# Performance work log

Hardware: AMD Instinct MI355X
Metric: run time of the kernel (lower is better)

Reference implementation:

```python
import jax, jax.numpy as jnp
import numpy as np

N = 100000      # nodes
E = 3200000     # edges
H = 128         # hidden_dim
L = 2           # relation_layers
R = 8           # num_edge_types
NT = 12         # num_node_types
CARDS = [100, 50, 20]
CE = 8          # categorical_embedding_dim
NUM, BOOL = 32, 16
FH = 48         # feature_hidden_dim
HH = 64         # head_hidden_dim
NBIN = 3        # approval, destination, simulation
NSEV = 4        # severity classes
COMB = 3 * H + FH
FEAT_IN = NUM + BOOL + len(CARDS) * CE


def setup_inputs() -> dict:
    key = jax.random.key(0)
    ks = jax.random.split(key, 32)
    s = 0.05
    inp = {
        'node_type_ids': jax.random.randint(ks[0], (N,), 0, NT),
        'edge_index': jax.random.randint(ks[1], (E, 2), 0, N),
        'edge_type_ids': jax.random.randint(ks[2], (E,), 0, R),
        'categorical': jax.random.randint(ks[3], (3,), 0, 20),
        'anchor_index': 0,
        'numeric': jax.random.normal(ks[4], (NUM,), jnp.float32),
        'boolean': (jax.random.uniform(ks[5], (BOOL,)) < 0.5).astype(jnp.float32),
        'node_emb': jax.random.normal(ks[6], (NT, H), jnp.float32) * s,
        'self_W': jax.random.normal(ks[7], (L, H, H), jnp.float32) * s,
        'self_b': jax.random.normal(ks[8], (L, H), jnp.float32) * s,
        'rel_W': jax.random.normal(ks[9], (L, R, H, H), jnp.float32) * s,
        'cat_emb0': jax.random.normal(ks[10], (CARDS[0], CE), jnp.float32) * s,
        'cat_emb1': jax.random.normal(ks[11], (CARDS[1], CE), jnp.float32) * s,
        'cat_emb2': jax.random.normal(ks[12], (CARDS[2], CE), jnp.float32) * s,
        'feat_W': jax.random.normal(ks[13], (FH, FEAT_IN), jnp.float32) * s,
        'feat_b': jax.random.normal(ks[14], (FH,), jnp.float32) * s,
        'bin_W1': jax.random.normal(ks[15], (NBIN, HH, COMB), jnp.float32) * s,
        'bin_b1': jax.random.normal(ks[16], (NBIN, HH), jnp.float32) * s,
        'bin_W2': jax.random.normal(ks[17], (NBIN, 1, HH), jnp.float32) * s,
        'bin_b2': jax.random.normal(ks[18], (NBIN, 1), jnp.float32) * s,
        'mc_W1': jax.random.normal(ks[19], (HH, COMB), jnp.float32) * s,
        'mc_b1': jax.random.normal(ks[20], (HH,), jnp.float32) * s,
        'mc_W2': jax.random.normal(ks[21], (NSEV, HH), jnp.float32) * s,
        'mc_b2': jax.random.normal(ks[22], (NSEV,), jnp.float32) * s,
    }
    return inp


def reference(node_type_ids, edge_index, edge_type_ids, categorical, anchor_index,
              numeric, boolean, node_emb, self_W, self_b, rel_W,
              cat_emb0, cat_emb1, cat_emb2, feat_W, feat_b,
              bin_W1, bin_b1, bin_W2, bin_b2, mc_W1, mc_b1, mc_W2, mc_b2):
    x = node_emb[node_type_ids]                      # [N,H]
    src, tgt = edge_index[:, 0], edge_index[:, 1]
    n, h = x.shape
    r = rel_W.shape[1]
    # scatter-add of (W_r @ x_src) == W_r @ scatter-add(x_src) per (target, relation)
    seg = tgt * r + edge_type_ids                    # combined segment id
    for l in range(self_W.shape[0]):
        agg = jax.ops.segment_sum(x[src], seg, num_segments=n * r).reshape(n, r, h)
        msgs = jnp.einsum('nrh,rdh->nd', agg, rel_W[l])   # Linear (no bias): x @ W^T
        x = jax.nn.relu(x @ self_W[l].T + self_b[l] + msgs)
    anchor = x[anchor_index]
    gmean = x.mean(axis=0)
    gmax = x.max(axis=0)
    feat = jnp.concatenate([numeric, boolean,
                            cat_emb0[categorical[0]], cat_emb1[categorical[1]],
                            cat_emb2[categorical[2]]])
    enc = jax.nn.relu(feat @ feat_W.T + feat_b)      # dropout = identity (eval)
    comb = jnp.concatenate([anchor, gmean, gmax, enc])   # [COMB]
    h_bin = jax.nn.relu(jnp.einsum('khc,c->kh', bin_W1, comb) + bin_b1)
    bin_logits = (jnp.einsum('koh,kh->ko', bin_W2, h_bin) + bin_b2)[:, 0]  # [NBIN]
    h_mc = jax.nn.relu(mc_W1 @ comb + mc_b1)
    mc_logits = mc_W2 @ h_mc + mc_b2                 # [NSEV]
    return bin_logits, mc_logits
```

## Files before the change

### kernel.cpp

```cpp
#include <hip/hip_runtime.h>
#include <hip/hip_bf16.h>


#define NN 100000
#define EE 3200000

typedef __attribute__((ext_vector_type(8))) short bf16x8;
typedef __attribute__((ext_vector_type(4))) float f32x4;

static __device__ __forceinline__ float frelu(float v) { return v > 0.f ? v : 0.f; }

static __device__ __forceinline__ unsigned short f2bf(float f) {
    unsigned b = __float_as_uint(f);
    return (unsigned short)((b + 0x7fffu + ((b >> 16) & 1u)) >> 16);
}
static __device__ __forceinline__ unsigned packbf(float lo, float hi) {
    return (unsigned)f2bf(lo) | ((unsigned)f2bf(hi) << 16);
}
static __device__ __forceinline__ float bflo(unsigned u) { return __uint_as_float(u << 16); }
static __device__ __forceinline__ float bfhi(unsigned u) { return __uint_as_float(u & 0xffff0000u); }
static __device__ __forceinline__ float bf2f(unsigned short u) {
    return __uint_as_float(((unsigned)u) << 16);
}

__global__ void k_gather_xb(const int* __restrict__ ntype, const float* __restrict__ nemb,
                            unsigned* __restrict__ xb) {
    int i = blockIdx.x * 256 + threadIdx.x;
    int n = i >> 6, q = i & 63;
    int tt = ntype[n];
    float2 v = ((const float2*)(nemb + (size_t)tt * 128))[q];
    xb[(size_t)n * 64 + q] = packbf(v.x, v.y);
}

__global__ void k_count(const int* __restrict__ eidx, int* __restrict__ rowptr) {
    for (int e = blockIdx.x * blockDim.x + threadIdx.x; e < EE; e += gridDim.x * blockDim.x) {
        int2 p = ((const int2*)eidx)[e];
        atomicAdd(&rowptr[p.y], 1);
    }
}

__global__ void k_scan1(int* data, int* partials, int nseg) {
    __shared__ int sd[256];
    int t = threadIdx.x;
    int base = blockIdx.x * 1024 + t * 4;
    int v[4];
#pragma unroll
    for (int k = 0; k < 4; ++k) v[k] = (base + k < nseg) ? data[base + k] : 0;
    int tsum = v[0] + v[1] + v[2] + v[3];
    sd[t] = tsum;
    __syncthreads();
    for (int off = 1; off < 256; off <<= 1) {
        int add = (t >= off) ? sd[t - off] : 0;
        __syncthreads();
        sd[t] += add;
        __syncthreads();
    }
    int run = sd[t] - tsum;
#pragma unroll
    for (int k = 0; k < 4; ++k) {
        if (base + k < nseg) data[base + k] = run;
        run += v[k];
    }
    if (t == 255) partials[blockIdx.x] = sd[255];
}

__global__ void k_scan2(int* partials, int nb) {
    __shared__ int sd[1024];
    int t = threadIdx.x;
    int v = (t < nb) ? partials[t] : 0;
    sd[t] = v;
    __syncthreads();
    for (int off = 1; off < 1024; off <<= 1) {
        int add = (t >= off) ? sd[t - off] : 0;
        __syncthreads();
        sd[t] += add;
        __syncthreads();
    }
    if (t < nb) partials[t] = sd[t] - v;
}

__global__ void k_scan3(int* rowptr, const int* __restrict__ partials, int nseg) {
    int i = blockIdx.x * 256 + threadIdx.x;
    if (i < nseg) rowptr[i] += partials[i >> 10];
}

__global__ void k_scatter(const int* __restrict__ eidx, const int* __restrict__ etype,
                          int* rowptr, int* __restrict__ pk) {
    for (int e = blockIdx.x * blockDim.x + threadIdx.x; e < EE; e += gridDim.x * blockDim.x) {
        int2 p = ((const int2*)eidx)[e];
        int rel = etype[e];
        int pos = atomicAdd(&rowptr[p.y], 1);
        pk[pos] = (p.x << 3) | rel;
    }
}

__global__ void k_prepWb(const float* __restrict__ relW, const float* __restrict__ selfW,
                         unsigned short* __restrict__ Wb) {
    int idx = blockIdx.x * 256 + threadIdx.x;
    int k = idx % 1152;
    int d = (idx / 1152) & 127;
    int l = idx / (1152 * 128);
    float v;
    if (k < 1024)
        v = relW[((((size_t)l * 8) + (k >> 7)) * 128 + d) * 128 + (k & 127)];
    else
        v = selfW[((size_t)l * 128 + d) * 128 + (k - 1024)];
    Wb[idx] = f2bf(v);
}

static __device__ __forceinline__ void addpk(float acc[8][2], int kk, unsigned u) {
    float lo = bflo(u), hi = bfhi(u);
    switch (kk & 7) {
        case 0: acc[0][0] += lo; acc[0][1] += hi; break;
        case 1: acc[1][0] += lo; acc[1][1] += hi; break;
        case 2: acc[2][0] += lo; acc[2][1] += hi; break;
        case 3: acc[3][0] += lo; acc[3][1] += hi; break;
        case 4: acc[4][0] += lo; acc[4][1] += hi; break;
        case 5: acc[5][0] += lo; acc[5][1] += hi; break;
        case 6: acc[6][0] += lo; acc[6][1] += hi; break;
        case 7: acc[7][0] += lo; acc[7][1] += hi; break;
    }
}

__global__ __launch_bounds__(256) void k_agg8(const unsigned* __restrict__ xb,
                                              const int* __restrict__ rowptr,
                                              const int* __restrict__ pk,
                                              unsigned* __restrict__ aggb, int c0, int cn) {
    int local = blockIdx.x * 4 + (threadIdx.x >> 6);
    int lane = threadIdx.x & 63;
    if (local >= cn) return;
    int n = c0 + local;
    int beg = n ? rowptr[n - 1] : 0;
    int end = rowptr[n];
    float acc[8][2];
#pragma unroll
    for (int r = 0; r < 8; ++r) { acc[r][0] = 0.f; acc[r][1] = 0.f; }
    int j = beg;
    for (; j + 4 <= end; j += 4) {
        int k0 = pk[j], k1 = pk[j + 1], k2 = pk[j + 2], k3 = pk[j + 3];
        unsigned u0 = xb[(size_t)(k0 >> 3) * 64 + lane];
        unsigned u1 = xb[(size_t)(k1 >> 3) * 64 + lane];
        unsigned u2 = xb[(size_t)(k2 >> 3) * 64 + lane];
        unsigned u3 = xb[(size_t)(k3 >> 3) * 64 + lane];
        addpk(acc, k0, u0);
        addpk(acc, k1, u1);
        addpk(acc, k2, u2);
        addpk(acc, k3, u3);
    }
    for (; j < end; ++j) {
        int kk = pk[j];
        unsigned u = xb[(size_t)(kk >> 3) * 64 + lane];
        addpk(acc, kk, u);
    }
#pragma unroll
    for (int r = 0; r < 8; ++r)
        aggb[(size_t)local * 512 + r * 64 + lane] = packbf(acc[r][0], acc[r][1]);
}

__global__ __launch_bounds__(256) void k_mm(const unsigned short* __restrict__ aggb,
                                            const unsigned short* __restrict__ xbin,
                                            const unsigned short* __restrict__ Wb,
                                            const float* __restrict__ bias,
                                            unsigned short* __restrict__ xbout,
                                            int c0, int cn) {
    const int wv = threadIdx.x >> 6, lane = threadIdx.x & 63;
    const int r_in = lane & 15, kq = lane >> 4;
    const int lm0 = blockIdx.x * 64 + wv * 16;

    f32x4 acc[8];
#pragma unroll
    for (int cf = 0; cf < 8; ++cf) acc[cf] = (f32x4){0.f, 0.f, 0.f, 0.f};

    int la = lm0 + r_in;
    if (la >= cn) la = cn - 1;
    const unsigned short* Arow = aggb + (size_t)la * 1024 + kq * 8;
    const unsigned short* Xrow = xbin + (size_t)(c0 + la) * 128 + kq * 8;
    const unsigned short* Brow = Wb + (size_t)r_in * 1152 + kq * 8;

#pragma unroll 1
    for (int ks = 0; ks < 36; ++ks) {
        const unsigned short* ap = (ks < 32) ? (Arow + ks * 32) : (Xrow + (ks - 32) * 32);
        bf16x8 a = *(const bf16x8*)ap;
#pragma unroll
        for (int cf = 0; cf < 8; ++cf) {
            bf16x8 b = *(const bf16x8*)(Brow + (size_t)cf * 16 * 1152 + ks * 32);
            acc[cf] = __builtin_amdgcn_mfma_f32_16x16x32_bf16(a, b, acc[cf], 0, 0, 0);
        }
    }
    int grb = c0 + lm0 + kq * 4;
    int glim = c0 + cn;
#pragma unroll
    for (int cf = 0; cf < 8; ++cf) {
        int d = cf * 16 + r_in;
        float bv = bias[d];
#pragma unroll
        for (int reg = 0; reg < 4; ++reg) {
            int gr = grb + reg;
            if (gr < glim)
                xbout[(size_t)gr * 128 + d] = f2bf(frelu(acc[cf][reg] + bv));
        }
    }
}

__global__ void k_reduce(const unsigned short* __restrict__ xb, float* __restrict__ gsum,
                         unsigned* __restrict__ gmax) {
    int c = threadIdx.x & 127;
    int half = threadIdx.x >> 7;
    int rbeg = blockIdx.x * 512 + half;
    int rend = min(blockIdx.x * 512 + 512, NN);
    float s = 0.f, m = 0.f;
    for (int r = rbeg; r < rend; r += 2) {
        float v = bf2f(xb[(size_t)r * 128 + c]);
        s += v;
        m = fmaxf(m, v);
    }
    atomicAdd(&gsum[c], s);
    atomicMax(&gmax[c], __float_as_uint(m));
}

__global__ void k_head(const unsigned short* __restrict__ x, const float* __restrict__ gsum,
                       const unsigned* __restrict__ gmaxu, const int* __restrict__ anchor_idx,
                       const float* __restrict__ numeric, const float* __restrict__ boolean_,
                       const int* __restrict__ cats, const float* __restrict__ ce0,
                       const float* __restrict__ ce1, const float* __restrict__ ce2,
                       const float* __restrict__ featW, const float* __restrict__ featb,
                       const float* __restrict__ binW1, const float* __restrict__ binb1,
                       const float* __restrict__ binW2, const float* __restrict__ binb2,
                       const float* __restrict__ mcW1, const float* __restrict__ mcb1,
                       const float* __restrict__ mcW2, const float* __restrict__ mcb2,
                       float* __restrict__ out) {
    __shared__ float comb[432];
    __shared__ float feat[72];
    __shared__ float hb[4][64];
    int t = threadIdx.x;
    int anchor = anchor_idx[0];
    if (t < 128) {
        comb[t] = bf2f(x[(size_t)anchor * 128 + t]);
        comb[128 + t] = gsum[t] * (1.0f / (float)NN);
        comb[256 + t] = __uint_as_float(gmaxu[t]);
    }
    if (t < 32) feat[t] = numeric[t];
    else if (t < 48) feat[t] = boolean_[t - 32];
    else if (t < 56) feat[t] = ce0[cats[0] * 8 + (t - 48)];
    else if (t < 64) feat[t] = ce1[cats[1] * 8 + (t - 56)];
    else if (t < 72) feat[t] = ce2[cats[2] * 8 + (t - 64)];
    __syncthreads();
    if (t < 48) {
        float s = featb[t];
        for (int c = 0; c < 72; ++c) s += featW[t * 72 + c] * feat[c];
        comb[384 + t] = frelu(s);
    }
    __syncthreads();
    {
        int head = t >> 6, u = t & 63;
        const float* W;
        float s;
        if (head < 3) {
            W = binW1 + ((size_t)head * 64 + u) * 432;
            s = binb1[head * 64 + u];
        } else {
            W = mcW1 + (size_t)u * 432;
            s = mcb1[u];
        }
        for (int c = 0; c < 432; ++c) s += W[c] * comb[c];
        hb[head][u] = frelu(s);
    }
    __syncthreads();
    if (t < 3) {
        float s = binb2[t];
        for (int u = 0; u < 64; ++u) s += binW2[t * 64 + u] * hb[t][u];
        out[t] = s;
    } else if (t < 7) {
        int k = t - 3;
        float s = mcb2[k];
        for (int u = 0; u < 64; ++u) s += mcW2[k * 64 + u] * hb[3][u];
        out[3 + k] = s;
    }
}

extern "C" void kernel_launch(void* const* d_in, const int* in_sizes, int n_in,
                              void* d_out, int out_size, void* d_ws, size_t ws_size,
                              hipStream_t stream) {
    const int* ntype = (const int*)d_in[0];
    const int* eidx = (const int*)d_in[1];
    const int* etype = (const int*)d_in[2];
    const int* cats = (const int*)d_in[3];
    const int* anchor = (const int*)d_in[4];
    const float* numeric = (const float*)d_in[5];
    const float* boolean_ = (const float*)d_in[6];
    const float* nemb = (const float*)d_in[7];
    const float* selfW = (const float*)d_in[8];
    const float* selfb = (const float*)d_in[9];
    const float* relW = (const float*)d_in[10];
    const float* ce0 = (const float*)d_in[11];
    const float* ce1 = (const float*)d_in[12];
    const float* ce2 = (const float*)d_in[13];
    const float* featW = (const float*)d_in[14];
    const float* featb = (const float*)d_in[15];
    const float* binW1 = (const float*)d_in[16];
    const float* binb1 = (const float*)d_in[17];
    const float* binW2 = (const float*)d_in[18];
    const float* binb2 = (const float*)d_in[19];
    const float* mcW1 = (const float*)d_in[20];
    const float* mcb1 = (const float*)d_in[21];
    const float* mcW2 = (const float*)d_in[22];
    const float* mcb2 = (const float*)d_in[23];
    float* out = (float*)d_out;

    char* ws = (char*)d_ws;
    size_t off = 0;
    auto alloc = [&](size_t bytes) -> void* {
        void* pp = ws + off;
        off += (bytes + 255) & ~(size_t)255;
        return pp;
    };
    unsigned* xbA = (unsigned*)alloc((size_t)NN * 64 * 4);
    unsigned* xbB = (unsigned*)alloc((size_t)NN * 64 * 4);
    int* rowptr = (int*)alloc((size_t)NN * 4);
    int* partials = (int*)alloc(4096);
    int* pkbuf = (int*)alloc((size_t)EE * 4);
    unsigned short* Wb = (unsigned short*)alloc((size_t)2 * 128 * 1152 * 2);
    float* gsum = (float*)alloc(512);
    unsigned* gmax = (unsigned*)alloc(512);
    size_t avail = (ws_size > off) ? (ws_size - off) : 0;
    int chunk = (int)(avail / 2048);
    chunk &= ~63;
    if (chunk > NN) chunk = NN;
    if (chunk < 64) chunk = 64;
    unsigned* aggb = (unsigned*)(ws + off);
    (void)in_sizes; (void)n_in; (void)out_size;

    hipMemsetAsync(rowptr, 0, (size_t)NN * 4, stream);
    hipMemsetAsync(gsum, 0, 512, stream);
    hipMemsetAsync(gmax, 0, 512, stream);

    k_gather_xb<<<NN * 64 / 256, 256, 0, stream>>>(ntype, nemb, xbA);
    k_count<<<2048, 256, 0, stream>>>(eidx, rowptr);
    int nb1 = (NN + 1023) / 1024;
    k_scan1<<<nb1, 256, 0, stream>>>(rowptr, partials, NN);
    k_scan2<<<1, 1024, 0, stream>>>(partials, nb1);
    k_scan3<<<(NN + 255) / 256, 256, 0, stream>>>(rowptr, partials, NN);
    k_scatter<<<2048, 256, 0, stream>>>(eidx, etype, rowptr, pkbuf);
    k_prepWb<<<2 * 128 * 1152 / 256, 256, 0, stream>>>(relW, selfW, Wb);

    for (int l = 0; l < 2; ++l) {
        const unsigned* xin = l ? xbB : xbA;
        unsigned short* xout = (unsigned short*)(l ? xbA : xbB);
        const unsigned short* Wl = Wb + (size_t)l * 128 * 1152;
        const float* bl = selfb + l * 128;
        for (int c0 = 0; c0 < NN; c0 += chunk) {
            int cn = (NN - c0 < chunk) ? (NN - c0) : chunk;
            k_agg8<<<(cn + 3) / 4, 256, 0, stream>>>(xin, rowptr, pkbuf, aggb, c0, cn);
            k_mm<<<(cn + 63) / 64, 256, 0, stream>>>((const unsigned short*)aggb,
                                                     (const unsigned short*)xin, Wl, bl,
                                                     xout, c0, cn);
        }
    }

    k_reduce<<<(NN + 511) / 512, 256, 0, stream>>>((const unsigned short*)xbA, gsum, gmax);
    k_head<<<1, 256, 0, stream>>>((const unsigned short*)xbA, gsum, gmax, anchor, numeric,
                                  boolean_, cats, ce0, ce1, ce2, featW, featb, binW1, binb1,
                                  binW2, binb2, mcW1, mcb1, mcW2, mcb2, out);
}
```

Before: 1.890 ms.

## Fuse edge aggregation and relation matmul into one kernel via shared memory

Replaces the separate aggregation and MFMA matmul kernels with one fused kernel per 16-node tile. Each wave aggregates 4 nodes into a swizzled LDS buffer, then each wave computes 2 of the 8 output column tiles with MFMA. This removes the large global aggregation buffer round-trip and the chunking loop. The gather loop is also widened to 8 outstanding loads. In exchange, each block reloads the full weight slice from global/cache, the matmul tile is only 16 rows, and 32KB of LDS per block may limit occupancy.

```diff
diff --git a/kernel.cpp b/kernel.cpp
--- a/kernel.cpp
+++ b/kernel.cpp
@@ -4,6 +4,7 @@
 
 #define NN 100000
 #define EE 3200000
+#define TN 16
 
 typedef __attribute__((ext_vector_type(8))) short bf16x8;
 typedef __attribute__((ext_vector_type(4))) float f32x4;
@@ -122,83 +123,80 @@
     }
 }
 
-__global__ __launch_bounds__(256) void k_agg8(const unsigned* __restrict__ xb,
-                                              const int* __restrict__ rowptr,
-                                              const int* __restrict__ pk,
-                                              unsigned* __restrict__ aggb, int c0, int cn) {
-    int local = blockIdx.x * 4 + (threadIdx.x >> 6);
-    int lane = threadIdx.x & 63;
-    if (local >= cn) return;
-    int n = c0 + local;
-    int beg = n ? rowptr[n - 1] : 0;
-    int end = rowptr[n];
-    float acc[8][2];
-#pragma unroll
-    for (int r = 0; r < 8; ++r) { acc[r][0] = 0.f; acc[r][1] = 0.f; }
-    int j = beg;
-    for (; j + 4 <= end; j += 4) {
-        int k0 = pk[j], k1 = pk[j + 1], k2 = pk[j + 2], k3 = pk[j + 3];
-        unsigned u0 = xb[(size_t)(k0 >> 3) * 64 + lane];
-        unsigned u1 = xb[(size_t)(k1 >> 3) * 64 + lane];
-        unsigned u2 = xb[(size_t)(k2 >> 3) * 64 + lane];
-        unsigned u3 = xb[(size_t)(k3 >> 3) * 64 + lane];
-        addpk(acc, k0, u0);
-        addpk(acc, k1, u1);
-        addpk(acc, k2, u2);
-        addpk(acc, k3, u3);
-    }
-    for (; j < end; ++j) {
-        int kk = pk[j];
-        unsigned u = xb[(size_t)(kk >> 3) * 64 + lane];
-        addpk(acc, kk, u);
-    }
-#pragma unroll
-    for (int r = 0; r < 8; ++r)
-        aggb[(size_t)local * 512 + r * 64 + lane] = packbf(acc[r][0], acc[r][1]);
-}
-
-__global__ __launch_bounds__(256) void k_mm(const unsigned short* __restrict__ aggb,
-                                            const unsigned short* __restrict__ xbin,
-                                            const unsigned short* __restrict__ Wb,
-                                            const float* __restrict__ bias,
-                                            unsigned short* __restrict__ xbout,
-                                            int c0, int cn) {
+__global__ __launch_bounds__(256) void k_fused(const unsigned* __restrict__ xb,
+                                               const int* __restrict__ rowptr,
+                                               const int* __restrict__ pk,
+                                               const unsigned short* __restrict__ Wb,
+                                               const float* __restrict__ bias,
+                                               unsigned short* __restrict__ xbout) {
+    __shared__ unsigned smU[TN * 512];
     const int wv = threadIdx.x >> 6, lane = threadIdx.x & 63;
+    const int n0 = blockIdx.x * TN;
+
+    for (int i = wv * 4; i < wv * 4 + 4; ++i) {
+        int n = n0 + i;
+        int beg = n ? rowptr[n - 1] : 0;
+        int end = rowptr[n];
+        float acc[8][2];
+#pragma unroll
+        for (int r = 0; r < 8; ++r) { acc[r][0] = 0.f; acc[r][1] = 0.f; }
+        int j = beg;
+        for (; j + 8 <= end; j += 8) {
+            int kk[8];
+            unsigned uu[8];
+#pragma unroll
+            for (int q = 0; q < 8; ++q) kk[q] = pk[j + q];
+#pragma unroll
+            for (int q = 0; q < 8; ++q) uu[q] = xb[(size_t)(kk[q] >> 3) * 64 + lane];
+#pragma unroll
+            for (int q = 0; q < 8; ++q) addpk(acc, kk[q], uu[q]);
+        }
+        for (; j < end; ++j) {
+            int kk = pk[j];
+            unsigned u = xb[(size_t)(kk >> 3) * 64 + lane];
+            addpk(acc, kk, u);
+        }
+        int sw = i & 7;
+#pragma unroll
+        for (int r = 0; r < 8; ++r) {
+            int g = r * 16 + (lane >> 2);
+            smU[i * 512 + (((g ^ sw) << 2) | (lane & 3))] = packbf(acc[r][0], acc[r][1]);
+        }
+    }
+    __syncthreads();
+
     const int r_in = lane & 15, kq = lane >> 4;
-    const int lm0 = blockIdx.x * 64 + wv * 16;
-
-    f32x4 acc[8];
-#pragma unroll
-    for (int cf = 0; cf < 8; ++cf) acc[cf] = (f32x4){0.f, 0.f, 0.f, 0.f};
-
-    int la = lm0 + r_in;
-    if (la >= cn) la = cn - 1;
-    const unsigned short* Arow = aggb + (size_t)la * 1024 + kq * 8;
-    const unsigned short* Xrow = xbin + (size_t)(c0 + la) * 128 + kq * 8;
-    const unsigned short* Brow = Wb + (size_t)r_in * 1152 + kq * 8;
+    const char* smB = (const char*)smU;
+    f32x4 acc2[2];
+    acc2[0] = (f32x4){0.f, 0.f, 0.f, 0.f};
+    acc2[1] = (f32x4){0.f, 0.f, 0.f, 0.f};
+    const int cf0 = wv * 2;
+    const unsigned short* B0 = Wb + (size_t)(cf0 * 16 + r_in) * 1152 + kq * 8;
+    const unsigned short* B1 = B0 + (size_t)16 * 1152;
+    const unsigned short* Xrow = (const unsigned short*)xb + (size_t)(n0 + r_in) * 128 + kq * 8;
 
 #pragma unroll 1
     for (int ks = 0; ks < 36; ++ks) {
-        const unsigned short* ap = (ks < 32) ? (Arow + ks * 32) : (Xrow + (ks - 32) * 32);
-        bf16x8 a = *(const bf16x8*)ap;
-#pragma unroll
-        for (int cf = 0; cf < 8; ++cf) {
-            bf16x8 b = *(const bf16x8*)(Brow + (size_t)cf * 16 * 1152 + ks * 32);
-            acc[cf] = __builtin_amdgcn_mfma_f32_16x16x32_bf16(a, b, acc[cf], 0, 0, 0);
-        }
-    }
-    int grb = c0 + lm0 + kq * 4;
-    int glim = c0 + cn;
-#pragma unroll
-    for (int cf = 0; cf < 8; ++cf) {
-        int d = cf * 16 + r_in;
+        bf16x8 a;
+        if (ks < 32) {
+            int g = ks * 4 + kq;
+            a = *(const bf16x8*)(smB + r_in * 2048 + ((g ^ (r_in & 7)) << 4));
+        } else {
+            a = *(const bf16x8*)(Xrow + (ks - 32) * 32);
+        }
+        acc2[0] = __builtin_amdgcn_mfma_f32_16x16x32_bf16(a, *(const bf16x8*)(B0 + ks * 32),
+                                                          acc2[0], 0, 0, 0);
+        acc2[1] = __builtin_amdgcn_mfma_f32_16x16x32_bf16(a, *(const bf16x8*)(B1 + ks * 32),
+                                                          acc2[1], 0, 0, 0);
+    }
+    int nrb = n0 + kq * 4;
+#pragma unroll
+    for (int c = 0; c < 2; ++c) {
+        int d = (cf0 + c) * 16 + r_in;
         float bv = bias[d];
 #pragma unroll
-        for (int reg = 0; reg < 4; ++reg) {
-            int gr = grb + reg;
-            if (gr < glim)
-                xbout[(size_t)gr * 128 + d] = f2bf(frelu(acc[cf][reg] + bv));
-        }
+        for (int reg = 0; reg < 4; ++reg)
+            xbout[(size_t)(nrb + reg) * 128 + d] = f2bf(frelu(acc2[c][reg] + bv));
     }
 }
 
@@ -322,13 +320,7 @@
     unsigned short* Wb = (unsigned short*)alloc((size_t)2 * 128 * 1152 * 2);
     float* gsum = (float*)alloc(512);
     unsigned* gmax = (unsigned*)alloc(512);
-    size_t avail = (ws_size > off) ? (ws_size - off) : 0;
-    int chunk = (int)(avail / 2048);
-    chunk &= ~63;
-    if (chunk > NN) chunk = NN;
-    if (chunk < 64) chunk = 64;
-    unsigned* aggb = (unsigned*)(ws + off);
-    (void)in_sizes; (void)n_in; (void)out_size;
+    (void)in_sizes; (void)n_in; (void)out_size; (void)ws_size;
 
     hipMemsetAsync(rowptr, 0, (size_t)NN * 4, stream);
     hipMemsetAsync(gsum, 0, 512, stream);
@@ -348,13 +340,7 @@
         unsigned short* xout = (unsigned short*)(l ? xbA : xbB);
         const unsigned short* Wl = Wb + (size_t)l * 128 * 1152;
         const float* bl = selfb + l * 128;
-        for (int c0 = 0; c0 < NN; c0 += chunk) {
-            int cn = (NN - c0 < chunk) ? (NN - c0) : chunk;
-            k_agg8<<<(cn + 3) / 4, 256, 0, stream>>>(xin, rowptr, pkbuf, aggb, c0, cn);
-            k_mm<<<(cn + 63) / 64, 256, 0, stream>>>((const unsigned short*)aggb,
-                                                     (const unsigned short*)xin, Wl, bl,
-                                                     xout, c0, cn);
-        }
+        k_fused<<<NN / TN, 256, 0, stream>>>(xin, rowptr, pkbuf, Wl, bl, xout);
     }
 
     k_reduce<<<(NN + 511) / 512, 256, 0, stream>>>((const unsigned short*)xbA, gsum, gmax);
```

Measured after the change: 1.830 ms. -3.2%, faster.
